# Kernel optimization log

Measured on AMD Instinct MI355X. Metric: run time of the kernel, lower is better.

Reference implementation:

```python
import jax, jax.numpy as jnp
import numpy as np

N = 20480      # total nodes
E = 327680     # total edges (avg degree 16)
B = 16         # graphs in batch
IN = 16        # node feature dim
H = 8          # hidden_out_channel
CO = 64        # conv_out_channel
ET = 36        # n_edge_types
EF = 2         # edge_features
OUT = 1        # classifier out
DIMS = [(IN, H), (H, H), (H, H), (H, CO)]


def setup_inputs() -> dict:
    key = jax.random.key(0)
    ks = jax.random.split(key, 32)
    inp = {}
    inp['x'] = jax.random.normal(ks[0], (N, IN), jnp.float32)
    inp['edge_index'] = jax.random.randint(ks[1], (2, E), 0, N)
    inp['edge_type'] = jax.random.randint(ks[2], (E,), 0, ET)
    inp['edge_attr'] = jax.random.normal(ks[3], (E, EF), jnp.float32)
    inp['cell_type'] = jax.random.randint(ks[4], (N,), 0, 2)
    inp['batch'] = (jnp.arange(N) // (N // B)).astype(jnp.int32)
    i = 5
    for l, (ci, co) in enumerate(DIMS, 1):
        d = ci * co
        s = 1.0 / np.sqrt(EF)
        inp[f'emb{l}'] = jax.random.normal(ks[i], (ET, d), jnp.float32) * 0.02; i += 1
        inp[f'wh{l}'] = jax.random.normal(ks[i], (EF, d), jnp.float32) * s; i += 1
        inp[f'bh{l}'] = jnp.zeros((d,), jnp.float32)
        inp[f'wg{l}'] = jax.random.normal(ks[i], (EF, d), jnp.float32) * s; i += 1
        inp[f'bg{l}'] = jnp.zeros((d,), jnp.float32)
        inp[f'root{l}'] = jax.random.normal(ks[i], (ci, co), jnp.float32) / np.sqrt(ci); i += 1
        inp[f'bias{l}'] = jnp.zeros((co,), jnp.float32)
    inp['clf_w'] = jax.random.normal(ks[i], (CO, OUT), jnp.float32) / np.sqrt(CO)
    inp['clf_b'] = jnp.zeros((OUT,), jnp.float32)
    return inp


def edge_weights(etype, ef, emb, wh, bh, wg, bg):
    # EdgeNN: relu(embedding(type) * fc_h(feat) + fc_g(feat)) -> [E, cin*cout]
    return jax.nn.relu(emb[etype] * (ef @ wh + bh) + (ef @ wg + bg))


def nnconv(h, src, dst, W, root, bias):
    # NNConv(aggr='mean', root_weight=True): gather src feats, per-edge matmul, scatter-mean
    cin, cout = root.shape
    msg = jnp.einsum('ei,eio->eo', h[src], W.reshape(-1, cin, cout))  # [E, cout]
    agg = jax.ops.segment_sum(msg, dst, num_segments=N)
    deg = jax.ops.segment_sum(jnp.ones_like(msg[:, 0]), dst, num_segments=N)
    return agg / jnp.maximum(deg, 1.0)[:, None] + h @ root + bias


def reference(x, edge_index, edge_type, edge_attr, cell_type, batch,
              emb1, wh1, bh1, wg1, bg1, root1, bias1,
              emb2, wh2, bh2, wg2, bg2, root2, bias2,
              emb3, wh3, bh3, wg3, bg3, root3, bias3,
              emb4, wh4, bh4, wg4, bg4, root4, bias4,
              clf_w, clf_b):
    src, dst = edge_index[0], edge_index[1]
    layers = [(emb1, wh1, bh1, wg1, bg1, root1, bias1),
              (emb2, wh2, bh2, wg2, bg2, root2, bias2),
              (emb3, wh3, bh3, wg3, bg3, root3, bias3),
              (emb4, wh4, bh4, wg4, bg4, root4, bias4)]
    h = x
    for (emb, wh, bh, wg, bg, root, bias) in layers:  # fixed 4 structurally-distinct layers
        W = edge_weights(edge_type, edge_attr, emb, wh, bh, wg, bg)
        h = jax.nn.relu(nnconv(h, src, dst, W, root, bias))
    # gated scatter-mean pooling over tumor cells (cell_type == 1)
    gate = (cell_type == 1).astype(jnp.int32)
    seg = gate * (batch.astype(jnp.int32) + 1)  # 0 = masked-out bucket
    pooled = jax.ops.segment_sum(h, seg, num_segments=B + 1)
    cnt = jax.ops.segment_sum(jnp.ones((h.shape[0],), h.dtype), seg, num_segments=B + 1)
    pooled = (pooled / jnp.maximum(cnt, 1.0)[:, None])[1:B + 1]  # [B, CO]
    return jax.nn.sigmoid(pooled @ clf_w + clf_b)  # hazards [B, OUT]
```

## Files before the change

kernel.cpp:

```cpp
#include <hip/hip_runtime.h>
#include <math.h>

#define NN 20480
#define NE 327680
#define NBATCH 16

typedef float v2f __attribute__((ext_vector_type(2)));

#if __has_builtin(__builtin_elementwise_max)
#define VMAX0(a) __builtin_elementwise_max((a), (v2f){0.f, 0.f})
#else
static __device__ __forceinline__ v2f VMAX0(v2f a) {
  v2f r; r.x = fmaxf(a.x, 0.f); r.y = fmaxf(a.y, 0.f); return r;
}
#endif

__global__ void hist_kernel(const int* __restrict__ dst, int* __restrict__ cnt) {
  int e = blockIdx.x * blockDim.x + threadIdx.x;
  if (e < NE) atomicAdd(&cnt[dst[e]], 1);
}

__global__ __launch_bounds__(1024) void scan_kernel(const int* __restrict__ cnt,
                                                    int* __restrict__ off) {
  __shared__ int part[1024];
  int tid = threadIdx.x;
  const int PT = NN / 1024;
  int loc[PT];
  int run = 0;
  int base = tid * PT;
#pragma unroll
  for (int k = 0; k < PT; k++) { loc[k] = run; run += cnt[base + k]; }
  part[tid] = run;
  __syncthreads();
  for (int d = 1; d < 1024; d <<= 1) {
    int t = (tid >= d) ? part[tid - d] : 0;
    __syncthreads();
    part[tid] += t;
    __syncthreads();
  }
  int pre = (tid == 0) ? 0 : part[tid - 1];
#pragma unroll
  for (int k = 0; k < PT; k++) off[base + k] = pre + loc[k];
  if (tid == 1023) off[NN] = pre + run;
}

__global__ void cursor_kernel(const int* __restrict__ off, int* __restrict__ cur) {
  int i = blockIdx.x * blockDim.x + threadIdx.x;
  if (i < NN) cur[i] = off[i];
}

__global__ void scatter_kernel(const int* __restrict__ src, const int* __restrict__ dst,
                               const int* __restrict__ etype, const float* __restrict__ eattr,
                               int* __restrict__ cur, float4* __restrict__ es) {
  int e = blockIdx.x * blockDim.x + threadIdx.x;
  if (e >= NE) return;
  int d = dst[e];
  int pos = atomicAdd(&cur[d], 1);
  es[pos] = make_float4(__int_as_float(src[e]), __int_as_float(etype[e]),
                        eattr[2 * e], eattr[2 * e + 1]);
}

template<int CIN>
__global__ __launch_bounds__(256) void layer_small(
    const int* __restrict__ off, const float4* __restrict__ es,
    const float* __restrict__ h_in,
    const float* __restrict__ emb, const float* __restrict__ wh,
    const float* __restrict__ bh, const float* __restrict__ wg,
    const float* __restrict__ bg,
    const float* __restrict__ root, const float* __restrict__ bias,
    float* __restrict__ h_out) {
  constexpr int D = CIN * 8;
  constexpr int S = D + 1;
  constexpr int P = CIN / 2;
  __shared__ float semb[36 * S];
  for (int idx = threadIdx.x; idx < 36 * D; idx += 256) {
    int t = idx / D, io = idx - t * D;
    semb[t * S + io] = emb[idx];
  }
  int lane = threadIdx.x & 63;
  int o = lane & 7, esub = lane >> 3;
  v2f rwh0[P], rwh1[P], rbh[P], rwg0[P], rwg1[P], rbg[P], rroot[P];
#pragma unroll
  for (int p = 0; p < P; p++) {
    int a = (2 * p) * 8 + o, b = (2 * p + 1) * 8 + o;
    rwh0[p] = (v2f){wh[a], wh[b]};
    rwh1[p] = (v2f){wh[D + a], wh[D + b]};
    rbh[p]  = (v2f){bh[a], bh[b]};
    rwg0[p] = (v2f){wg[a], wg[b]};
    rwg1[p] = (v2f){wg[D + a], wg[D + b]};
    rbg[p]  = (v2f){bg[a], bg[b]};
    rroot[p] = (v2f){root[a], root[b]};
  }
  float rbias = bias[o];
  __syncthreads();
  int wid = __builtin_amdgcn_readfirstlane(blockIdx.x * 4 + (threadIdx.x >> 6));
  for (int k = 0; k < 4; k++) {
    int n = wid * 4 + k;
    int beg = off[n], end = off[n + 1];
    float acc = 0.f;
    for (int j = beg + esub; j < end; j += 8) {
      float4 rec = es[j];
      int s = __float_as_int(rec.x);
      int t = __float_as_int(rec.y);
      v2f ef0 = (v2f){rec.z, rec.z}, ef1 = (v2f){rec.w, rec.w};
      const float4* hp = (const float4*)(h_in + s * CIN);
      const float* st = &semb[t * S + o];
      v2f msg = {0.f, 0.f};
#pragma unroll
      for (int q = 0; q < CIN / 4; q++) {
        float4 hv4 = hp[q];
        v2f hv0 = (v2f){hv4.x, hv4.y}, hv1 = (v2f){hv4.z, hv4.w};
        int p0 = 2 * q, p1 = 2 * q + 1;
        v2f hA = ef0 * rwh0[p0] + ef1 * rwh1[p0] + rbh[p0];
        v2f gA = ef0 * rwg0[p0] + ef1 * rwg1[p0] + rbg[p0];
        v2f sA = (v2f){st[(4 * q) * 8], st[(4 * q + 1) * 8]};
        msg += hv0 * VMAX0(sA * hA + gA);
        v2f hB = ef0 * rwh0[p1] + ef1 * rwh1[p1] + rbh[p1];
        v2f gB = ef0 * rwg0[p1] + ef1 * rwg1[p1] + rbg[p1];
        v2f sB = (v2f){st[(4 * q + 2) * 8], st[(4 * q + 3) * 8]};
        msg += hv1 * VMAX0(sB * hB + gB);
      }
      acc += msg.x + msg.y;
    }
    acc += __shfl_xor(acc, 8);
    acc += __shfl_xor(acc, 16);
    acc += __shfl_xor(acc, 32);
    float deg = (float)(end - beg);
    const float* hn = h_in + n * CIN;
    v2f rtv = {rbias, 0.f};
#pragma unroll
    for (int p = 0; p < P; p++)
      rtv += (v2f){hn[2 * p], hn[2 * p + 1]} * rroot[p];
    float val = fmaxf(rtv.x + rtv.y + acc / fmaxf(deg, 1.f), 0.f);
    if (lane < 8) h_out[n * 8 + o] = val;
  }
}

__global__ __launch_bounds__(512) void layer_l4(
    const int* __restrict__ off, const float4* __restrict__ es,
    const float* __restrict__ h_in,
    const float* __restrict__ emb, const float* __restrict__ wh,
    const float* __restrict__ bh, const float* __restrict__ wg,
    const float* __restrict__ bg,
    const float* __restrict__ root, const float* __restrict__ bias,
    float* __restrict__ h_out) {
  __shared__ float semb[36 * 512];
  {
    const float4* e4 = (const float4*)emb;
    float4* s4 = (float4*)semb;
    for (int idx = threadIdx.x; idx < 36 * 128; idx += 512) s4[idx] = e4[idx];
  }
  int lane = threadIdx.x & 63;
  v2f rwh0[4], rwh1[4], rbh[4], rwg0[4], rwg1[4], rbg[4], rroot[4];
#pragma unroll
  for (int p = 0; p < 4; p++) {
    int a = (2 * p) * 64 + lane, b = (2 * p + 1) * 64 + lane;
    rwh0[p] = (v2f){wh[a], wh[b]};
    rwh1[p] = (v2f){wh[512 + a], wh[512 + b]};
    rbh[p]  = (v2f){bh[a], bh[b]};
    rwg0[p] = (v2f){wg[a], wg[b]};
    rwg1[p] = (v2f){wg[512 + a], wg[512 + b]};
    rbg[p]  = (v2f){bg[a], bg[b]};
    rroot[p] = (v2f){root[a], root[b]};
  }
  float rbias = bias[lane];
  __syncthreads();
  int wid = __builtin_amdgcn_readfirstlane(blockIdx.x * 8 + (threadIdx.x >> 6));
  for (int k = 0; k < 4; k++) {
    int n = wid * 4 + k;
    int beg = off[n], end = off[n + 1];
    float acc = 0.f;
    for (int e = beg; e < end; ++e) {
      float4 rec = es[e];
      int s = __float_as_int(rec.x);
      int t = __float_as_int(rec.y);
      v2f ef0 = (v2f){rec.z, rec.z}, ef1 = (v2f){rec.w, rec.w};
      const float4* hp = (const float4*)(h_in + s * 8);
      float4 h0 = hp[0], h1 = hp[1];
      v2f hv[4] = {(v2f){h0.x, h0.y}, (v2f){h0.z, h0.w},
                   (v2f){h1.x, h1.y}, (v2f){h1.z, h1.w}};
      const float* st = &semb[t * 512 + lane];
      v2f msg = {0.f, 0.f};
#pragma unroll
      for (int p = 0; p < 4; p++) {
        v2f hval = ef0 * rwh0[p] + ef1 * rwh1[p] + rbh[p];
        v2f gval = ef0 * rwg0[p] + ef1 * rwg1[p] + rbg[p];
        v2f stv = (v2f){st[(2 * p) * 64], st[(2 * p + 1) * 64]};
        msg += hv[p] * VMAX0(stv * hval + gval);
      }
      acc += msg.x + msg.y;
    }
    float deg = (float)(end - beg);
    const float* hn = h_in + n * 8;
    v2f rtv = {rbias, 0.f};
#pragma unroll
    for (int p = 0; p < 4; p++)
      rtv += (v2f){hn[2 * p], hn[2 * p + 1]} * rroot[p];
    h_out[n * 64 + lane] = fmaxf(rtv.x + rtv.y + acc / fmaxf(deg, 1.f), 0.f);
  }
}

__global__ __launch_bounds__(256) void pool1_kernel(
    const float* __restrict__ h4, const int* __restrict__ ct,
    float* __restrict__ pooled, float* __restrict__ pcnt) {
  __shared__ float ss[4][64];
  __shared__ float sc[4];
  int b = blockIdx.x / 20, c = blockIdx.x % 20;
  int base = b * (NN / NBATCH) + c * 64;
  int o = threadIdx.x & 63, sub = threadIdx.x >> 6;
  float sum = 0.f, cnt = 0.f;
  for (int j = sub; j < 64; j += 4) {
    int n = base + j;
    if (ct[n] == 1) { sum += h4[n * 64 + o]; cnt += 1.f; }
  }
  ss[sub][o] = sum;
  if (o == 0) sc[sub] = cnt;
  __syncthreads();
  if (threadIdx.x < 64) {
    float tot = ss[0][o] + ss[1][o] + ss[2][o] + ss[3][o];
    unsafeAtomicAdd(&pooled[b * 64 + o], tot);
    if (o == 0) unsafeAtomicAdd(&pcnt[b], sc[0] + sc[1] + sc[2] + sc[3]);
  }
}

__global__ __launch_bounds__(1024) void pool2_kernel(
    const float* __restrict__ pooled, const float* __restrict__ pcnt,
    const float* __restrict__ clf_w, const float* __restrict__ clf_b,
    float* __restrict__ out) {
  int b = threadIdx.x >> 6, o = threadIdx.x & 63;
  float c = pcnt[b];
  float v = (pooled[b * 64 + o] / fmaxf(c, 1.f)) * clf_w[o];
#pragma unroll
  for (int d = 32; d; d >>= 1) v += __shfl_down(v, d);
  if (o == 0) out[b] = 1.f / (1.f + expf(-(v + clf_b[0])));
}

extern "C" void kernel_launch(void* const* d_in, const int* in_sizes, int n_in,
                              void* d_out, int out_size, void* d_ws, size_t ws_size,
                              hipStream_t stream) {
  (void)in_sizes; (void)n_in; (void)out_size; (void)ws_size;
  const float* x     = (const float*)d_in[0];
  const int*   eidx  = (const int*)d_in[1];
  const int*   src   = eidx;
  const int*   dst   = eidx + NE;
  const int*   etype = (const int*)d_in[2];
  const float* eattr = (const float*)d_in[3];
  const int*   ct    = (const int*)d_in[4];
  const float *emb[4], *wh[4], *bh[4], *wg[4], *bg[4], *root[4], *bias[4];
  for (int l = 0; l < 4; l++) {
    int b0 = 6 + 7 * l;
    emb[l]  = (const float*)d_in[b0 + 0];
    wh[l]   = (const float*)d_in[b0 + 1];
    bh[l]   = (const float*)d_in[b0 + 2];
    wg[l]   = (const float*)d_in[b0 + 3];
    bg[l]   = (const float*)d_in[b0 + 4];
    root[l] = (const float*)d_in[b0 + 5];
    bias[l] = (const float*)d_in[b0 + 6];
  }
  const float* clf_w = (const float*)d_in[34];
  const float* clf_b = (const float*)d_in[35];
  float* outp = (float*)d_out;

  float* ws  = (float*)d_ws;
  int*    off    = (int*)ws;
  float4* es     = (float4*)(ws + 20484);
  float*  hA     = ws + 20484 + 4 * NE;
  float*  hB     = hA + 8 * NN;
  float*  h4     = hB + 8 * NN;
  float*  pooled = h4 + 64 * NN;
  float*  pcnt   = pooled + 16 * 64;
  int*    cnt    = (int*)h4;
  int*    cur    = cnt + NN;

  hipMemsetAsync(cnt, 0, NN * sizeof(int), stream);
  hipMemsetAsync(pooled, 0, (16 * 64 + 16) * sizeof(float), stream);
  hist_kernel<<<NE / 256, 256, 0, stream>>>(dst, cnt);
  scan_kernel<<<1, 1024, 0, stream>>>(cnt, off);
  cursor_kernel<<<(NN + 255) / 256, 256, 0, stream>>>(off, cur);
  scatter_kernel<<<NE / 256, 256, 0, stream>>>(src, dst, etype, eattr, cur, es);

  layer_small<16><<<1280, 256, 0, stream>>>(off, es, x,
      emb[0], wh[0], bh[0], wg[0], bg[0], root[0], bias[0], hA);
  layer_small<8><<<1280, 256, 0, stream>>>(off, es, hA,
      emb[1], wh[1], bh[1], wg[1], bg[1], root[1], bias[1], hB);
  layer_small<8><<<1280, 256, 0, stream>>>(off, es, hB,
      emb[2], wh[2], bh[2], wg[2], bg[2], root[2], bias[2], hA);
  layer_l4<<<640, 512, 0, stream>>>(off, es, hA,
      emb[3], wh[3], bh[3], wg[3], bg[3], root[3], bias[3], h4);

  pool1_kernel<<<320, 256, 0, stream>>>(h4, ct, pooled, pcnt);
  pool2_kernel<<<1, 1024, 0, stream>>>(pooled, pcnt, clf_w, clf_b, outp);
}
```

Measured before the change: 328.8 us.

## Rebalance layer work split, drop LDS staging in layer 4, fuse cursor init

Layer 4 no longer stages its 72KB embedding table in LDS. It reads the table directly from global/L2 and uses one wave per node with two edges unrolled per iteration, launched as many small 256-thread blocks. This aims to lift the occupancy limit that the large shared buffer imposed. Layer 1 splits the 16 input channels across two lane halves so each wave handles two nodes instead of four. The cursor-copy kernel is folded into the scan kernel to save one launch. The trade-off is more global/cache traffic for embedding reads in layer 4 in exchange for higher occupancy and more parallelism.

```diff
diff --git a/kernel.cpp b/kernel.cpp
--- a/kernel.cpp
+++ b/kernel.cpp
@@ -21,7 +21,8 @@
 }
 
 __global__ __launch_bounds__(1024) void scan_kernel(const int* __restrict__ cnt,
-                                                    int* __restrict__ off) {
+                                                    int* __restrict__ off,
+                                                    int* __restrict__ cur) {
   __shared__ int part[1024];
   int tid = threadIdx.x;
   const int PT = NN / 1024;
@@ -40,13 +41,11 @@
   }
   int pre = (tid == 0) ? 0 : part[tid - 1];
 #pragma unroll
-  for (int k = 0; k < PT; k++) off[base + k] = pre + loc[k];
+  for (int k = 0; k < PT; k++) {
+    off[base + k] = pre + loc[k];
+    cur[base + k] = pre + loc[k];
+  }
   if (tid == 1023) off[NN] = pre + run;
-}
-
-__global__ void cursor_kernel(const int* __restrict__ off, int* __restrict__ cur) {
-  int i = blockIdx.x * blockDim.x + threadIdx.x;
-  if (i < NN) cur[i] = off[i];
 }
 
 __global__ void scatter_kernel(const int* __restrict__ src, const int* __restrict__ dst,
@@ -60,8 +59,7 @@
                         eattr[2 * e], eattr[2 * e + 1]);
 }
 
-template<int CIN>
-__global__ __launch_bounds__(256) void layer_small(
+__global__ __launch_bounds__(256) void layer_small16(
     const int* __restrict__ off, const float4* __restrict__ es,
     const float* __restrict__ h_in,
     const float* __restrict__ emb, const float* __restrict__ wh,
@@ -69,19 +67,93 @@
     const float* __restrict__ bg,
     const float* __restrict__ root, const float* __restrict__ bias,
     float* __restrict__ h_out) {
-  constexpr int D = CIN * 8;
+  constexpr int D = 128;
   constexpr int S = D + 1;
-  constexpr int P = CIN / 2;
   __shared__ float semb[36 * S];
   for (int idx = threadIdx.x; idx < 36 * D; idx += 256) {
     int t = idx / D, io = idx - t * D;
     semb[t * S + io] = emb[idx];
   }
   int lane = threadIdx.x & 63;
+  int o = lane & 7;
+  int ihalf = (lane >> 3) & 1;
+  int esub = lane >> 4;
+  int ibase = ihalf * 8;
+  v2f rwh0[4], rwh1[4], rbh[4], rwg0[4], rwg1[4], rbg[4], rroot[4];
+#pragma unroll
+  for (int p = 0; p < 4; p++) {
+    int a = (ibase + 2 * p) * 8 + o, b = (ibase + 2 * p + 1) * 8 + o;
+    rwh0[p] = (v2f){wh[a], wh[b]};
+    rwh1[p] = (v2f){wh[D + a], wh[D + b]};
+    rbh[p]  = (v2f){bh[a], bh[b]};
+    rwg0[p] = (v2f){wg[a], wg[b]};
+    rwg1[p] = (v2f){wg[D + a], wg[D + b]};
+    rbg[p]  = (v2f){bg[a], bg[b]};
+    rroot[p] = (v2f){root[a], root[b]};
+  }
+  float rbias = bias[o];
+  __syncthreads();
+  int wid = __builtin_amdgcn_readfirstlane(blockIdx.x * 4 + (threadIdx.x >> 6));
+  for (int k = 0; k < 2; k++) {
+    int n = wid * 2 + k;
+    int beg = off[n], end = off[n + 1];
+    float acc = 0.f;
+    for (int j = beg + esub; j < end; j += 4) {
+      float4 rec = es[j];
+      int s = __float_as_int(rec.x);
+      int t = __float_as_int(rec.y);
+      v2f ef0 = (v2f){rec.z, rec.z}, ef1 = (v2f){rec.w, rec.w};
+      const float4* hp = (const float4*)(h_in + s * 16 + ibase);
+      float4 h0 = hp[0], h1 = hp[1];
+      v2f hv[4] = {(v2f){h0.x, h0.y}, (v2f){h0.z, h0.w},
+                   (v2f){h1.x, h1.y}, (v2f){h1.z, h1.w}};
+      const float* st = &semb[t * S + ibase * 8 + o];
+      v2f msg = {0.f, 0.f};
+#pragma unroll
+      for (int p = 0; p < 4; p++) {
+        v2f hval = ef0 * rwh0[p] + ef1 * rwh1[p] + rbh[p];
+        v2f gval = ef0 * rwg0[p] + ef1 * rwg1[p] + rbg[p];
+        v2f stv = (v2f){st[(2 * p) * 8], st[(2 * p + 1) * 8]};
+        msg += hv[p] * VMAX0(stv * hval + gval);
+      }
+      acc += msg.x + msg.y;
+    }
+    acc += __shfl_xor(acc, 8);
+    acc += __shfl_xor(acc, 16);
+    acc += __shfl_xor(acc, 32);
+    const float* hn = h_in + n * 16 + ibase;
+    v2f rtv = {0.f, 0.f};
+#pragma unroll
+    for (int p = 0; p < 4; p++)
+      rtv += (v2f){hn[2 * p], hn[2 * p + 1]} * rroot[p];
+    float rt = rtv.x + rtv.y;
+    rt += __shfl_xor(rt, 8);
+    float deg = (float)(end - beg);
+    float val = fmaxf(rbias + rt + acc / fmaxf(deg, 1.f), 0.f);
+    if (lane < 8) h_out[n * 8 + o] = val;
+  }
+}
+
+__global__ __launch_bounds__(256) void layer_small8(
+    const int* __restrict__ off, const float4* __restrict__ es,
+    const float* __restrict__ h_in,
+    const float* __restrict__ emb, const float* __restrict__ wh,
+    const float* __restrict__ bh, const float* __restrict__ wg,
+    const float* __restrict__ bg,
+    const float* __restrict__ root, const float* __restrict__ bias,
+    float* __restrict__ h_out) {
+  constexpr int D = 64;
+  constexpr int S = D + 1;
+  __shared__ float semb[36 * S];
+  for (int idx = threadIdx.x; idx < 36 * D; idx += 256) {
+    int t = idx / D, io = idx - t * D;
+    semb[t * S + io] = emb[idx];
+  }
+  int lane = threadIdx.x & 63;
   int o = lane & 7, esub = lane >> 3;
-  v2f rwh0[P], rwh1[P], rbh[P], rwg0[P], rwg1[P], rbg[P], rroot[P];
-#pragma unroll
-  for (int p = 0; p < P; p++) {
+  v2f rwh0[4], rwh1[4], rbh[4], rwg0[4], rwg1[4], rbg[4], rroot[4];
+#pragma unroll
+  for (int p = 0; p < 4; p++) {
     int a = (2 * p) * 8 + o, b = (2 * p + 1) * 8 + o;
     rwh0[p] = (v2f){wh[a], wh[b]};
     rwh1[p] = (v2f){wh[D + a], wh[D + b]};
@@ -103,22 +175,18 @@
       int s = __float_as_int(rec.x);
       int t = __float_as_int(rec.y);
       v2f ef0 = (v2f){rec.z, rec.z}, ef1 = (v2f){rec.w, rec.w};
-      const float4* hp = (const float4*)(h_in + s * CIN);
+      const float4* hp = (const float4*)(h_in + s * 8);
+      float4 h0 = hp[0], h1 = hp[1];
+      v2f hv[4] = {(v2f){h0.x, h0.y}, (v2f){h0.z, h0.w},
+                   (v2f){h1.x, h1.y}, (v2f){h1.z, h1.w}};
       const float* st = &semb[t * S + o];
       v2f msg = {0.f, 0.f};
 #pragma unroll
-      for (int q = 0; q < CIN / 4; q++) {
-        float4 hv4 = hp[q];
-        v2f hv0 = (v2f){hv4.x, hv4.y}, hv1 = (v2f){hv4.z, hv4.w};
-        int p0 = 2 * q, p1 = 2 * q + 1;
-        v2f hA = ef0 * rwh0[p0] + ef1 * rwh1[p0] + rbh[p0];
-        v2f gA = ef0 * rwg0[p0] + ef1 * rwg1[p0] + rbg[p0];
-        v2f sA = (v2f){st[(4 * q) * 8], st[(4 * q + 1) * 8]};
-        msg += hv0 * VMAX0(sA * hA + gA);
-        v2f hB = ef0 * rwh0[p1] + ef1 * rwh1[p1] + rbh[p1];
-        v2f gB = ef0 * rwg0[p1] + ef1 * rwg1[p1] + rbg[p1];
-        v2f sB = (v2f){st[(4 * q + 2) * 8], st[(4 * q + 3) * 8]};
-        msg += hv1 * VMAX0(sB * hB + gB);
+      for (int p = 0; p < 4; p++) {
+        v2f hval = ef0 * rwh0[p] + ef1 * rwh1[p] + rbh[p];
+        v2f gval = ef0 * rwg0[p] + ef1 * rwg1[p] + rbg[p];
+        v2f stv = (v2f){st[(2 * p) * 8], st[(2 * p + 1) * 8]};
+        msg += hv[p] * VMAX0(stv * hval + gval);
       }
       acc += msg.x + msg.y;
     }
@@ -126,17 +194,17 @@
     acc += __shfl_xor(acc, 16);
     acc += __shfl_xor(acc, 32);
     float deg = (float)(end - beg);
-    const float* hn = h_in + n * CIN;
-    v2f rtv = {rbias, 0.f};
-#pragma unroll
-    for (int p = 0; p < P; p++)
+    const float* hn = h_in + n * 8;
+    v2f rtv = {0.f, 0.f};
+#pragma unroll
+    for (int p = 0; p < 4; p++)
       rtv += (v2f){hn[2 * p], hn[2 * p + 1]} * rroot[p];
-    float val = fmaxf(rtv.x + rtv.y + acc / fmaxf(deg, 1.f), 0.f);
+    float val = fmaxf(rbias + rtv.x + rtv.y + acc / fmaxf(deg, 1.f), 0.f);
     if (lane < 8) h_out[n * 8 + o] = val;
   }
 }
 
-__global__ __launch_bounds__(512) void layer_l4(
+__global__ __launch_bounds__(256) void layer_l4(
     const int* __restrict__ off, const float4* __restrict__ es,
     const float* __restrict__ h_in,
     const float* __restrict__ emb, const float* __restrict__ wh,
@@ -144,12 +212,6 @@
     const float* __restrict__ bg,
     const float* __restrict__ root, const float* __restrict__ bias,
     float* __restrict__ h_out) {
-  __shared__ float semb[36 * 512];
-  {
-    const float4* e4 = (const float4*)emb;
-    float4* s4 = (float4*)semb;
-    for (int idx = threadIdx.x; idx < 36 * 128; idx += 512) s4[idx] = e4[idx];
-  }
   int lane = threadIdx.x & 63;
   v2f rwh0[4], rwh1[4], rbh[4], rwg0[4], rwg1[4], rbg[4], rroot[4];
 #pragma unroll
@@ -164,40 +226,71 @@
     rroot[p] = (v2f){root[a], root[b]};
   }
   float rbias = bias[lane];
-  __syncthreads();
-  int wid = __builtin_amdgcn_readfirstlane(blockIdx.x * 8 + (threadIdx.x >> 6));
-  for (int k = 0; k < 4; k++) {
-    int n = wid * 4 + k;
-    int beg = off[n], end = off[n + 1];
-    float acc = 0.f;
-    for (int e = beg; e < end; ++e) {
-      float4 rec = es[e];
-      int s = __float_as_int(rec.x);
-      int t = __float_as_int(rec.y);
-      v2f ef0 = (v2f){rec.z, rec.z}, ef1 = (v2f){rec.w, rec.w};
-      const float4* hp = (const float4*)(h_in + s * 8);
-      float4 h0 = hp[0], h1 = hp[1];
-      v2f hv[4] = {(v2f){h0.x, h0.y}, (v2f){h0.z, h0.w},
-                   (v2f){h1.x, h1.y}, (v2f){h1.z, h1.w}};
-      const float* st = &semb[t * 512 + lane];
-      v2f msg = {0.f, 0.f};
-#pragma unroll
-      for (int p = 0; p < 4; p++) {
-        v2f hval = ef0 * rwh0[p] + ef1 * rwh1[p] + rbh[p];
-        v2f gval = ef0 * rwg0[p] + ef1 * rwg1[p] + rbg[p];
-        v2f stv = (v2f){st[(2 * p) * 64], st[(2 * p + 1) * 64]};
-        msg += hv[p] * VMAX0(stv * hval + gval);
-      }
-      acc += msg.x + msg.y;
+  int n = __builtin_amdgcn_readfirstlane(blockIdx.x * 4 + (threadIdx.x >> 6));
+  int beg = off[n], end = off[n + 1];
+  float acc0 = 0.f, acc1 = 0.f;
+  int e = beg;
+  for (; e + 2 <= end; e += 2) {
+    float4 r0 = es[e], r1 = es[e + 1];
+    int s0 = __float_as_int(r0.x), t0 = __float_as_int(r0.y);
+    int s1 = __float_as_int(r1.x), t1 = __float_as_int(r1.y);
+    const float4* hp0 = (const float4*)(h_in + s0 * 8);
+    const float4* hp1 = (const float4*)(h_in + s1 * 8);
+    float4 a0 = hp0[0], a1 = hp0[1];
+    float4 b0 = hp1[0], b1 = hp1[1];
+    const float* st0 = emb + t0 * 512 + lane;
+    const float* st1 = emb + t1 * 512 + lane;
+    v2f sv0[4], sv1[4];
+#pragma unroll
+    for (int p = 0; p < 4; p++) sv0[p] = (v2f){st0[(2 * p) * 64], st0[(2 * p + 1) * 64]};
+#pragma unroll
+    for (int p = 0; p < 4; p++) sv1[p] = (v2f){st1[(2 * p) * 64], st1[(2 * p + 1) * 64]};
+    v2f hva[4] = {(v2f){a0.x, a0.y}, (v2f){a0.z, a0.w},
+                  (v2f){a1.x, a1.y}, (v2f){a1.z, a1.w}};
+    v2f hvb[4] = {(v2f){b0.x, b0.y}, (v2f){b0.z, b0.w},
+                  (v2f){b1.x, b1.y}, (v2f){b1.z, b1.w}};
+    v2f e00 = (v2f){r0.z, r0.z}, e01 = (v2f){r0.w, r0.w};
+    v2f e10 = (v2f){r1.z, r1.z}, e11 = (v2f){r1.w, r1.w};
+    v2f m0 = {0.f, 0.f}, m1 = {0.f, 0.f};
+#pragma unroll
+    for (int p = 0; p < 4; p++) {
+      v2f hv0 = e00 * rwh0[p] + e01 * rwh1[p] + rbh[p];
+      v2f gv0 = e00 * rwg0[p] + e01 * rwg1[p] + rbg[p];
+      m0 += hva[p] * VMAX0(sv0[p] * hv0 + gv0);
+      v2f hv1 = e10 * rwh0[p] + e11 * rwh1[p] + rbh[p];
+      v2f gv1 = e10 * rwg0[p] + e11 * rwg1[p] + rbg[p];
+      m1 += hvb[p] * VMAX0(sv1[p] * hv1 + gv1);
     }
-    float deg = (float)(end - beg);
-    const float* hn = h_in + n * 8;
-    v2f rtv = {rbias, 0.f};
-#pragma unroll
-    for (int p = 0; p < 4; p++)
-      rtv += (v2f){hn[2 * p], hn[2 * p + 1]} * rroot[p];
-    h_out[n * 64 + lane] = fmaxf(rtv.x + rtv.y + acc / fmaxf(deg, 1.f), 0.f);
-  }
+    acc0 += m0.x + m0.y;
+    acc1 += m1.x + m1.y;
+  }
+  if (e < end) {
+    float4 r0 = es[e];
+    int s0 = __float_as_int(r0.x), t0 = __float_as_int(r0.y);
+    const float4* hp0 = (const float4*)(h_in + s0 * 8);
+    float4 a0 = hp0[0], a1 = hp0[1];
+    const float* st0 = emb + t0 * 512 + lane;
+    v2f hva[4] = {(v2f){a0.x, a0.y}, (v2f){a0.z, a0.w},
+                  (v2f){a1.x, a1.y}, (v2f){a1.z, a1.w}};
+    v2f e00 = (v2f){r0.z, r0.z}, e01 = (v2f){r0.w, r0.w};
+    v2f m0 = {0.f, 0.f};
+#pragma unroll
+    for (int p = 0; p < 4; p++) {
+      v2f hv0 = e00 * rwh0[p] + e01 * rwh1[p] + rbh[p];
+      v2f gv0 = e00 * rwg0[p] + e01 * rwg1[p] + rbg[p];
+      v2f stv = (v2f){st0[(2 * p) * 64], st0[(2 * p + 1) * 64]};
+      m0 += hva[p] * VMAX0(stv * hv0 + gv0);
+    }
+    acc0 += m0.x + m0.y;
+  }
+  float acc = acc0 + acc1;
+  float deg = (float)(end - beg);
+  const float* hn = h_in + n * 8;
+  v2f rtv = {0.f, 0.f};
+#pragma unroll
+  for (int p = 0; p < 4; p++)
+    rtv += (v2f){hn[2 * p], hn[2 * p + 1]} * rroot[p];
+  h_out[n * 64 + lane] = fmaxf(rbias + rtv.x + rtv.y + acc / fmaxf(deg, 1.f), 0.f);
 }
 
 __global__ __launch_bounds__(256) void pool1_kernel(
@@ -275,17 +368,16 @@
   hipMemsetAsync(cnt, 0, NN * sizeof(int), stream);
   hipMemsetAsync(pooled, 0, (16 * 64 + 16) * sizeof(float), stream);
   hist_kernel<<<NE / 256, 256, 0, stream>>>(dst, cnt);
-  scan_kernel<<<1, 1024, 0, stream>>>(cnt, off);
-  cursor_kernel<<<(NN + 255) / 256, 256, 0, stream>>>(off, cur);
+  scan_kernel<<<1, 1024, 0, stream>>>(cnt, off, cur);
   scatter_kernel<<<NE / 256, 256, 0, stream>>>(src, dst, etype, eattr, cur, es);
 
-  layer_small<16><<<1280, 256, 0, stream>>>(off, es, x,
+  layer_small16<<<2560, 256, 0, stream>>>(off, es, x,
       emb[0], wh[0], bh[0], wg[0], bg[0], root[0], bias[0], hA);
-  layer_small<8><<<1280, 256, 0, stream>>>(off, es, hA,
+  layer_small8<<<1280, 256, 0, stream>>>(off, es, hA,
       emb[1], wh[1], bh[1], wg[1], bg[1], root[1], bias[1], hB);
-  layer_small<8><<<1280, 256, 0, stream>>>(off, es, hB,
+  layer_small8<<<1280, 256, 0, stream>>>(off, es, hB,
       emb[2], wh[2], bh[2], wg[2], bg[2], root[2], bias[2], hA);
-  layer_l4<<<640, 512, 0, stream>>>(off, es, hA,
+  layer_l4<<<5120, 256, 0, stream>>>(off, es, hA,
       emb[3], wh[3], bh[3], wg[3], bg[3], root[3], bias[3], h4);
 
   pool1_kernel<<<320, 256, 0, stream>>>(h4, ct, pooled, pcnt);
```

Result: faster. 298.6 us (-9.2%).
